# Kernel tuning notes

Hardware: AMD Instinct MI355X
Metric: run time of the kernel (lower is better)

The kernel has to match this reference:

```python
import jax, jax.numpy as jnp
import numpy as np

N_NODES = 100000
N_EDGES = 1000000
D = 128


def setup_inputs() -> dict:
    key = jax.random.key(0)
    k1, k2, k3, k4 = jax.random.split(key, 4)
    x = jax.random.normal(k1, (N_NODES, D), dtype=jnp.float32)
    src = jax.random.randint(k2, (N_EDGES,), 0, N_NODES, dtype=jnp.int64)
    dst = jax.random.randint(k3, (N_EDGES,), 0, N_NODES, dtype=jnp.int64)
    # nn.Linear(2*D, 1): weight [1, 2*D], bias [1]
    W = jax.random.normal(k4, (1, 2 * D), dtype=jnp.float32) / np.sqrt(2 * D)
    b = jnp.zeros((1,), dtype=jnp.float32)
    return {"x": x, "src": src, "dst": dst, "W": W, "b": b}


def reference(x, src, dst, W, b):
    # cat([x[src], x[dst]], 1) @ W.T + b  ==  x[src] @ w_s + x[dst] @ w_d + b
    w_s = W[0, :D]   # [D]
    w_d = W[0, D:]   # [D]
    logits = x[src] @ w_s + x[dst] @ w_d + b[0]  # [E]
    return jax.nn.sigmoid(logits)  # squeezed score per edge
```

## Files before the change

kernel.cpp:

```cpp
#include <hip/hip_runtime.h>
#include <math.h>


#define DIM 128

__global__ __launch_bounds__(256) void proj_kernel(
    const float* __restrict__ x,
    const float* __restrict__ W,
    float* __restrict__ ps,
    float* __restrict__ pd,
    int n_nodes)
{
    const int half = threadIdx.x >> 5;
    const int lane = threadIdx.x & 31;
    const int node = blockIdx.x * 8 + half;
    if (node >= n_nodes) return;

    const float4* x4 = (const float4*)x + (size_t)node * (DIM / 4) + lane;
    float4 v = *x4;

    const float4* w4 = (const float4*)W;
    float4 ws = w4[lane];
    float4 wd = w4[32 + lane];

    float s = v.x * ws.x + v.y * ws.y + v.z * ws.z + v.w * ws.w;
    float d = v.x * wd.x + v.y * wd.y + v.z * wd.z + v.w * wd.w;

    #pragma unroll
    for (int off = 16; off > 0; off >>= 1) {
        s += __shfl_down(s, off, 32);
        d += __shfl_down(d, off, 32);
    }
    if (lane == 0) {
        ps[node] = s;
        pd[node] = d;
    }
}

__global__ __launch_bounds__(256) void edge_kernel(
    const int* __restrict__ src,
    const int* __restrict__ dst,
    const float* __restrict__ ps,
    const float* __restrict__ pd,
    const float* __restrict__ b,
    float* __restrict__ out,
    int n_edges)
{
    const int e = blockIdx.x * blockDim.x + threadIdx.x;
    if (e >= n_edges) return;
    const float z = ps[src[e]] + pd[dst[e]] + b[0];
    out[e] = 1.0f / (1.0f + __expf(-z));
}

extern "C" void kernel_launch(void* const* d_in, const int* in_sizes, int n_in,
                              void* d_out, int out_size, void* d_ws, size_t ws_size,
                              hipStream_t stream) {
    const float* x   = (const float*)d_in[0];
    const int*   src = (const int*)d_in[1];
    const int*   dst = (const int*)d_in[2];
    const float* W   = (const float*)d_in[3];
    const float* b   = (const float*)d_in[4];
    float* out = (float*)d_out;

    const int n_nodes = in_sizes[0] / DIM;
    const int n_edges = in_sizes[1];

    float* ps = (float*)d_ws;
    float* pd = ps + n_nodes;

    proj_kernel<<<(n_nodes + 7) / 8, 256, 0, stream>>>(x, W, ps, pd, n_nodes);
    edge_kernel<<<(n_edges + 255) / 256, 256, 0, stream>>>(src, dst, ps, pd, b, out, n_edges);
}
```

Baseline: 102.9 us.

## Grid-stride projection with two nodes per iteration and vectorized edge kernel

The projection kernel becomes a fixed 2048-block grid-stride loop in which each 32-lane group handles two nodes per iteration, putting two row loads in flight at once. The edge kernel is rebuilt to read src/dst as int4 and write float4 outputs, processing four edges per thread, with a separate tail kernel for any leftover edges. Together these aim to raise memory-level parallelism and cut per-element instruction overhead. The cost is fewer resident threads in the projection pass and an extra launch when the edge count is not a multiple of four.

```diff
diff --git a/kernel.cpp b/kernel.cpp
--- a/kernel.cpp
+++ b/kernel.cpp
@@ -3,6 +3,10 @@
 
 
 #define DIM 128
+
+__device__ __forceinline__ float sigmoidf_fast(float z) {
+    return 1.0f / (1.0f + __expf(-z));
+}
 
 __global__ __launch_bounds__(256) void proj_kernel(
     const float* __restrict__ x,
@@ -11,45 +15,85 @@
     float* __restrict__ pd,
     int n_nodes)
 {
-    const int half = threadIdx.x >> 5;
-    const int lane = threadIdx.x & 31;
-    const int node = blockIdx.x * 8 + half;
-    if (node >= n_nodes) return;
-
-    const float4* x4 = (const float4*)x + (size_t)node * (DIM / 4) + lane;
-    float4 v = *x4;
+    const int lane    = threadIdx.x & 31;
+    const int half_id = (blockIdx.x * blockDim.x + threadIdx.x) >> 5;
+    const int n_half  = (gridDim.x * blockDim.x) >> 5;
 
     const float4* w4 = (const float4*)W;
-    float4 ws = w4[lane];
-    float4 wd = w4[32 + lane];
+    const float4 ws = w4[lane];
+    const float4 wd = w4[32 + lane];
+    const float4* x4 = (const float4*)x;
 
-    float s = v.x * ws.x + v.y * ws.y + v.z * ws.z + v.w * ws.w;
-    float d = v.x * wd.x + v.y * wd.y + v.z * wd.z + v.w * wd.w;
-
-    #pragma unroll
-    for (int off = 16; off > 0; off >>= 1) {
-        s += __shfl_down(s, off, 32);
-        d += __shfl_down(d, off, 32);
+    int node = half_id;
+    for (; node + n_half < n_nodes; node += 2 * n_half) {
+        const int n0 = node, n1 = node + n_half;
+        float4 v0 = x4[(size_t)n0 * 32 + lane];
+        float4 v1 = x4[(size_t)n1 * 32 + lane];
+        float s0 = v0.x*ws.x + v0.y*ws.y + v0.z*ws.z + v0.w*ws.w;
+        float d0 = v0.x*wd.x + v0.y*wd.y + v0.z*wd.z + v0.w*wd.w;
+        float s1 = v1.x*ws.x + v1.y*ws.y + v1.z*ws.z + v1.w*ws.w;
+        float d1 = v1.x*wd.x + v1.y*wd.y + v1.z*wd.z + v1.w*wd.w;
+        #pragma unroll
+        for (int off = 16; off > 0; off >>= 1) {
+            s0 += __shfl_down(s0, off, 32);
+            d0 += __shfl_down(d0, off, 32);
+            s1 += __shfl_down(s1, off, 32);
+            d1 += __shfl_down(d1, off, 32);
+        }
+        if (lane == 0) {
+            ps[n0] = s0; pd[n0] = d0;
+            ps[n1] = s1; pd[n1] = d1;
+        }
     }
-    if (lane == 0) {
-        ps[node] = s;
-        pd[node] = d;
+    if (node < n_nodes) {
+        float4 v = x4[(size_t)node * 32 + lane];
+        float s = v.x*ws.x + v.y*ws.y + v.z*ws.z + v.w*ws.w;
+        float d = v.x*wd.x + v.y*wd.y + v.z*wd.z + v.w*wd.w;
+        #pragma unroll
+        for (int off = 16; off > 0; off >>= 1) {
+            s += __shfl_down(s, off, 32);
+            d += __shfl_down(d, off, 32);
+        }
+        if (lane == 0) { ps[node] = s; pd[node] = d; }
     }
 }
 
-__global__ __launch_bounds__(256) void edge_kernel(
+__global__ __launch_bounds__(256) void edge_kernel4(
+    const int4* __restrict__ src4,
+    const int4* __restrict__ dst4,
+    const float* __restrict__ ps,
+    const float* __restrict__ pd,
+    const float* __restrict__ b,
+    float4* __restrict__ out4,
+    int n_quads)
+{
+    const int i = blockIdx.x * blockDim.x + threadIdx.x;
+    if (i >= n_quads) return;
+    const int4 s = src4[i];
+    const int4 d = dst4[i];
+    const float bb = b[0];
+    float a0 = ps[s.x], a1 = ps[s.y], a2 = ps[s.z], a3 = ps[s.w];
+    float c0 = pd[d.x], c1 = pd[d.y], c2 = pd[d.z], c3 = pd[d.w];
+    float4 o;
+    o.x = sigmoidf_fast(a0 + c0 + bb);
+    o.y = sigmoidf_fast(a1 + c1 + bb);
+    o.z = sigmoidf_fast(a2 + c2 + bb);
+    o.w = sigmoidf_fast(a3 + c3 + bb);
+    out4[i] = o;
+}
+
+__global__ __launch_bounds__(64) void edge_kernel_tail(
     const int* __restrict__ src,
     const int* __restrict__ dst,
     const float* __restrict__ ps,
     const float* __restrict__ pd,
     const float* __restrict__ b,
     float* __restrict__ out,
-    int n_edges)
+    int start, int n_edges)
 {
-    const int e = blockIdx.x * blockDim.x + threadIdx.x;
+    const int e = start + blockIdx.x * blockDim.x + threadIdx.x;
     if (e >= n_edges) return;
-    const float z = ps[src[e]] + pd[dst[e]] + b[0];
-    out[e] = 1.0f / (1.0f + __expf(-z));
+    out[e] = sigmoidf_fast(ps[src[e]] + pd[dst[e]] + b[0]);
 }
 
 extern "C" void kernel_launch(void* const* d_in, const int* in_sizes, int n_in,
@@ -68,6 +112,17 @@
     float* ps = (float*)d_ws;
     float* pd = ps + n_nodes;
 
-    proj_kernel<<<(n_nodes + 7) / 8, 256, 0, stream>>>(x, W, ps, pd, n_nodes);
-    edge_kernel<<<(n_edges + 255) / 256, 256, 0, stream>>>(src, dst, ps, pd, b, out, n_edges);
+    proj_kernel<<<2048, 256, 0, stream>>>(x, W, ps, pd, n_nodes);
+
+    const int n_quads = n_edges / 4;
+    if (n_quads > 0) {
+        edge_kernel4<<<(n_quads + 255) / 256, 256, 0, stream>>>(
+            (const int4*)src, (const int4*)dst, ps, pd, b, (float4*)out, n_quads);
+    }
+    const int tail_start = n_quads * 4;
+    const int n_tail = n_edges - tail_start;
+    if (n_tail > 0) {
+        edge_kernel_tail<<<(n_tail + 63) / 64, 64, 0, stream>>>(
+            src, dst, ps, pd, b, out, tail_start, n_edges);
+    }
 }
```

Result: no change. 104.0 us (+1.0%).
